# Kernel optimization log

Hardware: AMD Instinct MI355X
Metric: run time of the kernel (lower is better)

The kernel has to match this reference:

```python
import jax, jax.numpy as jnp
import numpy as np
from jax import lax

# L segments, N candidate spans per segment, S words per segment,
# MAX_W max span width, K spans kept, D_EMB = 3*768 span emb, D_HID ffnn hidden
L, N, S, MAX_W, K, D_EMB, D_HID = 8, 7168, 256, 30, 128, 2304, 150


def setup_inputs():
    key = jax.random.key(0)
    k0, k1, k2, k3, k4 = jax.random.split(key, 5)
    span_emb = jax.random.normal(k0, (L, N, D_EMB), dtype=jnp.float32)
    W1 = jax.random.normal(k1, (D_EMB, D_HID), dtype=jnp.float32) * 0.02
    b1 = jnp.zeros((D_HID,), jnp.float32)
    W2 = jax.random.normal(k2, (D_HID, 1), dtype=jnp.float32) * 0.02
    b2 = jnp.zeros((1,), jnp.float32)
    starts = jax.random.randint(k3, (L, N), 0, S - MAX_W, dtype=jnp.int32)
    widths = jax.random.randint(k4, (L, N), 0, MAX_W, dtype=jnp.int32)
    ends = starts + widths  # valid spans: start <= end < S, width < MAX_W
    return {"span_emb": span_emb, "W1": W1, "b1": b1, "W2": W2, "b2": b2,
            "candidate_starts": starts, "candidate_ends": ends,
            "num_output_spans": K, "max_sentence_length": S}


def _extract_one(scores, starts, ends, k_out, max_len):
    """Greedy non-crossing span selection for one segment (ExtractSpans, sort_spans=True).

    latest_end[j]   = latest end among selected spans starting at j   (init -1)
    earliest_start[j] = earliest start among selected spans ending at j (init +inf)
    A candidate (s,e) crosses a selected span iff exists j in (s,e] with
    latest_end[j] > e, or j in [s,e) with earliest_start[j] < s.
    """
    pad = max_len + MAX_W + 1
    order = jnp.argsort(-scores).astype(jnp.int32)  # descending by score
    s_srt, e_srt = starts[order], ends[order]
    offs = jnp.arange(MAX_W + 1, dtype=jnp.int32)

    def step(carry, xs):
        le, es, sel, n = carry
        i, s, e = xs
        win_le = lax.dynamic_slice(le, (s,), (MAX_W + 1,))  # j = s .. s+MAX_W
        win_es = lax.dynamic_slice(es, (s,), (MAX_W + 1,))
        w = e - s
        crossing = jnp.any((offs >= 1) & (offs <= w) & (win_le > e)) | \
                   jnp.any((offs < w) & (win_es < s))
        take = jnp.logical_and(~crossing, n < k_out)
        nc = jnp.minimum(n, k_out - 1)
        sel = sel.at[nc].set(jnp.where(take, i, sel[nc]))
        le = le.at[s].set(jnp.where(take, jnp.maximum(le[s], e), le[s]))
        es = es.at[e].set(jnp.where(take, jnp.minimum(es[e], s), es[e]))
        return (le, es, sel, n + take.astype(jnp.int32)), None

    init = (jnp.full((pad,), -1, jnp.int32),
            jnp.full((pad,), pad, jnp.int32),
            jnp.zeros((k_out,), jnp.int32),
            jnp.int32(0))
    (le, es, sel, n), _ = lax.scan(step, init, (order, s_srt, e_srt))

    # sort_spans=True: reorder selected spans by (start, end); pad tail with first.
    slot = jnp.arange(k_out, dtype=jnp.int32)
    sortkey = jnp.where(slot < n, starts[sel] * pad + ends[sel], jnp.int32(2**31 - 1))
    sel_sorted = sel[jnp.argsort(sortkey)]
    return jnp.where(slot < n, sel_sorted, sel_sorted[0])


def reference(span_emb, W1, b1, W2, b2, candidate_starts, candidate_ends,
              num_output_spans, max_sentence_length):
    # FFNN mention scoring (ffnn_m: Linear -> ReLU -> Linear, output size 1)
    h = jax.nn.relu(jnp.einsum('lnd,dh->lnh', span_emb, W1) + b1)
    scores = (jnp.einsum('lnh,ho->lno', h, W2) + b2)[..., 0]  # [L, N]
    idx = jax.vmap(lambda sc, st, en: _extract_one(sc, st, en,
                                                   num_output_spans,
                                                   max_sentence_length))(
        scores, candidate_starts, candidate_ends)  # [L, K] int32
    sel_scores = jnp.take_along_axis(scores, idx, axis=1)  # [L, K]
    return sel_scores, idx
```

## Files before the change

### kernel.cpp

```cpp
#include <hip/hip_runtime.h>
#include <stdint.h>

#define LSEG 8
#define NCAND 7168
#define SLEN 256
#define MAXW 30
#define KOUT 128
#define DEMB 2304
#define DHID 150
#define PADV (SLEN + MAXW + 1)

__global__ __launch_bounds__(256) void k_transpose(const float* __restrict__ w1,
                                                   float* __restrict__ w1t) {
    int i = blockIdx.x * 256 + threadIdx.x;
    if (i < DHID * DEMB) {
        int n = i / DEMB;
        int k = i - n * DEMB;
        w1t[i] = w1[k * DHID + n];
    }
}

__global__ __launch_bounds__(256, 2) void k_scores(
    const float* __restrict__ emb, const float* __restrict__ w1t,
    const float* __restrict__ b1, const float* __restrict__ w2,
    const float* __restrict__ b2, float* __restrict__ scores) {
    __shared__ float smem[64 * 68 + 160 * 68];
    float* amem = smem;
    float* wmem = smem + 64 * 68;

    const int tid = threadIdx.x;
    const int tx = tid & 15;
    const int ty = tid >> 4;
    const int M0 = blockIdx.x * 64;

    for (int i = tid; i < 10 * 68; i += 256) wmem[150 * 68 + i] = 0.f;

    float acc[4][10];
#pragma unroll
    for (int i = 0; i < 4; ++i) {
#pragma unroll
        for (int j = 0; j < 10; ++j) acc[i][j] = 0.f;
    }

    for (int k0 = 0; k0 < DEMB; k0 += 64) {
        __syncthreads();
#pragma unroll
        for (int r = 0; r < 4; ++r) {
            int m = ty + 16 * r;
            float4 v = *(const float4*)(emb + (size_t)(M0 + m) * DEMB + k0 + tx * 4);
            *(float4*)(amem + m * 68 + tx * 4) = v;
        }
        for (int c = tid; c < 2400; c += 256) {
            int n = c >> 4, q = c & 15;
            float4 v = *(const float4*)(w1t + (size_t)n * DEMB + k0 + q * 4);
            *(float4*)(wmem + n * 68 + q * 4) = v;
        }
        __syncthreads();
#pragma unroll 4
        for (int kk = 0; kk < 64; kk += 4) {
            float4 av[4];
            float4 wv[10];
#pragma unroll
            for (int i = 0; i < 4; ++i)
                av[i] = *(const float4*)(amem + (ty * 4 + i) * 68 + kk);
#pragma unroll
            for (int j = 0; j < 10; ++j)
                wv[j] = *(const float4*)(wmem + (tx + 16 * j) * 68 + kk);
#pragma unroll
            for (int i = 0; i < 4; ++i) {
#pragma unroll
                for (int j = 0; j < 10; ++j) {
                    acc[i][j] += av[i].x * wv[j].x;
                    acc[i][j] += av[i].y * wv[j].y;
                    acc[i][j] += av[i].z * wv[j].z;
                    acc[i][j] += av[i].w * wv[j].w;
                }
            }
        }
    }

    float partial[4] = {0.f, 0.f, 0.f, 0.f};
#pragma unroll
    for (int j = 0; j < 10; ++j) {
        int n = tx + 16 * j;
        float bb = (n < DHID) ? b1[n] : 0.f;
        float ww = (n < DHID) ? w2[n] : 0.f;
#pragma unroll
        for (int i = 0; i < 4; ++i) {
            float h = acc[i][j] + bb;
            h = fmaxf(h, 0.f);
            partial[i] += h * ww;
        }
    }
    __syncthreads();
    float* red = smem;
#pragma unroll
    for (int i = 0; i < 4; ++i) red[(ty * 4 + i) * 17 + tx] = partial[i];
    __syncthreads();
    if (tid < 64) {
        float sacc = 0.f;
#pragma unroll
        for (int t = 0; t < 16; ++t) sacc += red[tid * 17 + t];
        scores[M0 + tid] = sacc + b2[0];
    }
}

__global__ __launch_bounds__(1024) void k_extract(
    const float* __restrict__ scores,
    const int* __restrict__ cs, const int* __restrict__ ce,
    float* __restrict__ out_sc, float* __restrict__ out_idx) {
    __shared__ unsigned ks[8192];
    __shared__ unsigned short id[8192];
    __shared__ int le[352];
    __shared__ int es[352];
    __shared__ int sel_idx[KOUT];
    __shared__ unsigned sel_se[KOUT];
    __shared__ unsigned skey[KOUT];
    __shared__ int nshare;

    const int tid = threadIdx.x;
    const int l = blockIdx.x;
    const int base = l * NCAND;

    for (int i = tid; i < 352; i += 1024) { le[i] = -1; es[i] = PADV; }
    if (tid < KOUT) { sel_idx[tid] = 0; sel_se[tid] = 0; }

    for (int t = tid; t < 8192; t += 1024) {
        if (t < NCAND) {
            unsigned u = __float_as_uint(scores[base + t]);
            u = (u & 0x80000000u) ? ~u : (u | 0x80000000u);
            ks[t] = ~u;
            id[t] = (unsigned short)t;
        } else {
            ks[t] = 0xFFFFFFFFu;
            id[t] = 0xFFFFu;
        }
    }

    for (int k = 2; k <= 8192; k <<= 1) {
        for (int j = k >> 1; j > 0; j >>= 1) {
            __syncthreads();
            for (int t = tid; t < 8192; t += 1024) {
                int p = t ^ j;
                if (p > t) {
                    unsigned ka = ks[t], kb = ks[p];
                    unsigned short ia = id[t], ib = id[p];
                    bool agtb = (ka > kb) || (ka == kb && ia > ib);
                    bool up = ((t & k) == 0);
                    if (agtb == up) {
                        ks[t] = kb; ks[p] = ka;
                        id[t] = ib; id[p] = ia;
                    }
                }
            }
        }
    }
    __syncthreads();

    for (int t = tid; t < NCAND; t += 1024) {
        int i0 = id[t];
        ks[t] = (unsigned)cs[base + i0] | ((unsigned)ce[base + i0] << 16);
    }
    __syncthreads();

    if (tid < 64) {
        volatile unsigned* ksv = ks;
        volatile int* lev = le;
        volatile int* esv = es;
        const int lane = tid;
        int n = 0;
        for (int t = 0; t < NCAND; ++t) {
            if (n >= KOUT) break;
            unsigned se = ksv[t];
            int s = (int)(se & 0xFFFFu);
            int e = (int)(se >> 16);
            int w = e - s;
            int ro = (lane <= MAXW) ? lane : 0;
            int lv = lev[s + ro];
            int ev = esv[s + ro];
            bool c1 = (lane >= 1) && (lane <= w) && (lv > e);
            bool c2 = (lane < w) && (ev < s);
            bool crossing = (__ballot(c1 || c2) != 0ull);
            if (!crossing) {
                if (lane == 0) {
                    sel_idx[n] = (int)id[t];
                    sel_se[n] = se;
                    if (e > lev[s]) lev[s] = e;
                    if (s < esv[e]) esv[e] = s;
                }
                n++;
            }
            __threadfence_block();
        }
        if (lane == 0) nshare = n;
    }
    __syncthreads();

    const int nsel = nshare;
    if (tid < KOUT) {
        if (tid < nsel) {
            unsigned se = sel_se[tid];
            int s = (int)(se & 0xFFFFu);
            int e = (int)(se >> 16);
            skey[tid] = ((unsigned)(s * PADV + e) << 7) | (unsigned)tid;
        } else {
            skey[tid] = 0x7F000000u | (unsigned)tid;
        }
    }
    for (int k = 2; k <= KOUT; k <<= 1) {
        for (int j = k >> 1; j > 0; j >>= 1) {
            __syncthreads();
            if (tid < KOUT) {
                int t = tid, p = t ^ j;
                if (p > t) {
                    unsigned a = skey[t], b = skey[p];
                    bool up = ((t & k) == 0);
                    if ((a > b) == up) { skey[t] = b; skey[p] = a; }
                }
            }
        }
    }
    __syncthreads();
    if (tid < KOUT) {
        int oslot = (int)(skey[tid] & 127u);
        int slot0 = (int)(skey[0] & 127u);
        int oi = (tid < nsel) ? sel_idx[oslot] : sel_idx[slot0];
        out_idx[l * KOUT + tid] = (float)oi;
        out_sc[l * KOUT + tid] = scores[base + oi];
    }
}

extern "C" void kernel_launch(void* const* d_in, const int* in_sizes, int n_in,
                              void* d_out, int out_size, void* d_ws, size_t ws_size,
                              hipStream_t stream) {
    const float* emb = (const float*)d_in[0];
    const float* w1  = (const float*)d_in[1];
    const float* b1  = (const float*)d_in[2];
    const float* w2  = (const float*)d_in[3];
    const float* b2  = (const float*)d_in[4];
    const int*   cs  = (const int*)d_in[5];
    const int*   ce  = (const int*)d_in[6];

    float* ws_scores = (float*)d_ws;
    float* ws_w1t    = (float*)((char*)d_ws + 262144);

    k_transpose<<<dim3(1350), dim3(256), 0, stream>>>(w1, ws_w1t);
    k_scores<<<dim3((LSEG * NCAND) / 64), dim3(256), 0, stream>>>(
        emb, ws_w1t, b1, w2, b2, ws_scores);
    k_extract<<<dim3(LSEG), dim3(1024), 0, stream>>>(
        ws_scores, cs, ce, (float*)d_out, (float*)d_out + LSEG * KOUT);
}
```

Measured before the change: 1.605 ms.

## Enlarge GEMM tile with direct-to-LDS swizzled loads and batch greedy span selection

The scoring GEMM now uses 112-row tiles with a 32-wide K step. Tiles are loaded with global_load_lds into an XOR-swizzled LDS layout, replacing the register-staged, padded copies. Separately, the greedy extraction now tests 64 sorted candidates per wavefront iteration against the current state, then resolves conflicts within the batch serially using ballot and shuffle. This aims to cut the per-candidate serial latency of the 7168-step loop, but adds more register pressure in the GEMM (7x10 accumulators) and relies on the batch conflict check matching the exact greedy semantics.

New measurement: 1.390 ms. -13.4%, faster.

```diff
diff --git a/kernel.cpp b/kernel.cpp
--- a/kernel.cpp
+++ b/kernel.cpp
@@ -10,6 +10,17 @@
 #define DHID 150
 #define PADV (SLEN + MAXW + 1)
 
+#define MTILE 112
+#define NPAD 160
+#define KT 32
+
+typedef const unsigned int __attribute__((address_space(1)))* gp_t;
+typedef unsigned int __attribute__((address_space(3)))* lp_t;
+
+__device__ __forceinline__ void gload16(const float* g, float* l) {
+    __builtin_amdgcn_global_load_lds((gp_t)g, (lp_t)l, 16, 0, 0);
+}
+
 __global__ __launch_bounds__(256) void k_transpose(const float* __restrict__ w1,
                                                    float* __restrict__ w1t) {
     int i = blockIdx.x * 256 + threadIdx.x;
@@ -24,50 +35,60 @@
     const float* __restrict__ emb, const float* __restrict__ w1t,
     const float* __restrict__ b1, const float* __restrict__ w2,
     const float* __restrict__ b2, float* __restrict__ scores) {
-    __shared__ float smem[64 * 68 + 160 * 68];
+    __shared__ float smem[(MTILE + NPAD) * KT];
     float* amem = smem;
-    float* wmem = smem + 64 * 68;
+    float* wmem = smem + MTILE * KT;
 
     const int tid = threadIdx.x;
     const int tx = tid & 15;
     const int ty = tid >> 4;
-    const int M0 = blockIdx.x * 64;
-
-    for (int i = tid; i < 10 * 68; i += 256) wmem[150 * 68 + i] = 0.f;
-
-    float acc[4][10];
-#pragma unroll
-    for (int i = 0; i < 4; ++i) {
+    const int M0 = blockIdx.x * MTILE;
+
+    for (int u = tid; u < (NPAD - DHID) * KT; u += 256) wmem[DHID * KT + u] = 0.f;
+
+    float acc[7][10];
+#pragma unroll
+    for (int i = 0; i < 7; ++i)
 #pragma unroll
         for (int j = 0; j < 10; ++j) acc[i][j] = 0.f;
-    }
-
-    for (int k0 = 0; k0 < DEMB; k0 += 64) {
+
+    for (int k0 = 0; k0 < DEMB; k0 += KT) {
+#pragma unroll
+        for (int r = 0; r < 4; ++r) {
+            int u = tid + 256 * r;
+            if (u < MTILE * 8) {
+                int row = u >> 3, cd = u & 7;
+                int gc = cd ^ (row & 7);
+                gload16(emb + (size_t)(M0 + row) * DEMB + k0 + gc * 4, amem + u * 4);
+            }
+        }
+#pragma unroll
+        for (int r = 0; r < 5; ++r) {
+            int u = tid + 256 * r;
+            if (u < DHID * 8) {
+                int row = u >> 3, cd = u & 7;
+                int gc = cd ^ (row & 7);
+                gload16(w1t + (size_t)row * DEMB + k0 + gc * 4, wmem + u * 4);
+            }
+        }
         __syncthreads();
-#pragma unroll
-        for (int r = 0; r < 4; ++r) {
-            int m = ty + 16 * r;
-            float4 v = *(const float4*)(emb + (size_t)(M0 + m) * DEMB + k0 + tx * 4);
-            *(float4*)(amem + m * 68 + tx * 4) = v;
-        }
-        for (int c = tid; c < 2400; c += 256) {
-            int n = c >> 4, q = c & 15;
-            float4 v = *(const float4*)(w1t + (size_t)n * DEMB + k0 + q * 4);
-            *(float4*)(wmem + n * 68 + q * 4) = v;
-        }
-        __syncthreads();
-#pragma unroll 4
-        for (int kk = 0; kk < 64; kk += 4) {
-            float4 av[4];
+
+#pragma unroll 2
+        for (int kc = 0; kc < 8; ++kc) {
+            float4 av[7];
             float4 wv[10];
 #pragma unroll
-            for (int i = 0; i < 4; ++i)
-                av[i] = *(const float4*)(amem + (ty * 4 + i) * 68 + kk);
-#pragma unroll
-            for (int j = 0; j < 10; ++j)
-                wv[j] = *(const float4*)(wmem + (tx + 16 * j) * 68 + kk);
-#pragma unroll
-            for (int i = 0; i < 4; ++i) {
+            for (int i = 0; i < 7; ++i) {
+                int row = ty * 7 + i;
+                av[i] = *(const float4*)(amem + row * KT + ((kc ^ (row & 7)) << 2));
+            }
+#pragma unroll
+            for (int j = 0; j < 10; ++j) {
+                int n = tx + 16 * j;
+                wv[j] = *(const float4*)(wmem + n * KT + ((kc ^ (tx & 7)) << 2));
+            }
+#pragma unroll
+            for (int i = 0; i < 7; ++i) {
 #pragma unroll
                 for (int j = 0; j < 10; ++j) {
                     acc[i][j] += av[i].x * wv[j].x;
@@ -77,27 +98,29 @@
                 }
             }
         }
-    }
-
-    float partial[4] = {0.f, 0.f, 0.f, 0.f};
+        __syncthreads();
+    }
+
+    float partial[7];
+#pragma unroll
+    for (int i = 0; i < 7; ++i) partial[i] = 0.f;
 #pragma unroll
     for (int j = 0; j < 10; ++j) {
         int n = tx + 16 * j;
         float bb = (n < DHID) ? b1[n] : 0.f;
         float ww = (n < DHID) ? w2[n] : 0.f;
 #pragma unroll
-        for (int i = 0; i < 4; ++i) {
+        for (int i = 0; i < 7; ++i) {
             float h = acc[i][j] + bb;
             h = fmaxf(h, 0.f);
             partial[i] += h * ww;
         }
     }
-    __syncthreads();
     float* red = smem;
 #pragma unroll
-    for (int i = 0; i < 4; ++i) red[(ty * 4 + i) * 17 + tx] = partial[i];
-    __syncthreads();
-    if (tid < 64) {
+    for (int i = 0; i < 7; ++i) red[(ty * 7 + i) * 17 + tx] = partial[i];
+    __syncthreads();
+    if (tid < MTILE) {
         float sacc = 0.f;
 #pragma unroll
         for (int t = 0; t < 16; ++t) sacc += red[tid * 17 + t];
@@ -164,31 +187,47 @@
     __syncthreads();
 
     if (tid < 64) {
-        volatile unsigned* ksv = ks;
         volatile int* lev = le;
         volatile int* esv = es;
         const int lane = tid;
         int n = 0;
-        for (int t = 0; t < NCAND; ++t) {
-            if (n >= KOUT) break;
-            unsigned se = ksv[t];
-            int s = (int)(se & 0xFFFFu);
-            int e = (int)(se >> 16);
-            int w = e - s;
-            int ro = (lane <= MAXW) ? lane : 0;
-            int lv = lev[s + ro];
-            int ev = esv[s + ro];
-            bool c1 = (lane >= 1) && (lane <= w) && (lv > e);
-            bool c2 = (lane < w) && (ev < s);
-            bool crossing = (__ballot(c1 || c2) != 0ull);
-            if (!crossing) {
-                if (lane == 0) {
-                    sel_idx[n] = (int)id[t];
-                    sel_se[n] = se;
-                    if (e > lev[s]) lev[s] = e;
-                    if (s < esv[e]) esv[e] = s;
-                }
-                n++;
+        for (int t0 = 0; t0 < NCAND && n < KOUT; t0 += 64) {
+            const int t = t0 + lane;
+            const unsigned se = ks[t];
+            const int s = (int)(se & 0xFFFFu);
+            const int e = (int)(se >> 16);
+            const int w = e - s;
+            bool cr = false;
+#pragma unroll
+            for (int ro = 0; ro <= MAXW; ++ro) {
+                int lv = lev[s + ro];
+                int ev = esv[s + ro];
+                cr = cr || ((ro >= 1) && (ro <= w) && (lv > e));
+                cr = cr || ((ro < w) && (ev < s));
+            }
+            unsigned long long ok = __ballot(!cr);
+            unsigned long long taken = 0ull;
+            const int nbase = n;
+            while (ok) {
+                int j = __builtin_ctzll(ok);
+                ok &= ok - 1ull;
+                int sj = __shfl(s, j);
+                int ej = __shfl(e, j);
+                bool crj = (s < sj && sj <= e && e < ej) ||
+                           (sj < s && s <= ej && ej < e);
+                unsigned long long cm = __ballot(crj);
+                if ((cm & taken) == 0ull) {
+                    taken |= (1ull << j);
+                    ++n;
+                    if (n >= KOUT) break;
+                }
+            }
+            if ((taken >> lane) & 1ull) {
+                int slot = nbase + __popcll(taken & ((1ull << lane) - 1ull));
+                sel_idx[slot] = (int)id[t];
+                sel_se[slot] = se;
+                atomicMax(&le[s], e);
+                atomicMin(&es[e], s);
             }
             __threadfence_block();
         }
@@ -245,7 +284,7 @@
     float* ws_w1t    = (float*)((char*)d_ws + 262144);
 
     k_transpose<<<dim3(1350), dim3(256), 0, stream>>>(w1, ws_w1t);
-    k_scores<<<dim3((LSEG * NCAND) / 64), dim3(256), 0, stream>>>(
+    k_scores<<<dim3((LSEG * NCAND) / MTILE), dim3(256), 0, stream>>>(
         emb, ws_w1t, b1, w2, b2, ws_scores);
     k_extract<<<dim3(LSEG), dim3(1024), 0, stream>>>(
         ws_scores, cs, ce, (float*)d_out, (float*)d_out + LSEG * KOUT);
```
